# Kernel optimization log

Hardware: AMD Instinct MI355X
Metric: run time of the kernel (lower is better)

The kernel has to match this reference:

```python
import jax, jax.numpy as jnp
import numpy as np

E = 512      # moe_experts
M = 6        # per-expert dim = moe_dim // 2
H = 6        # moe_heads
D = 1024     # hidden_size
F = E * M    # flatten_shape = 3072

def relu2(x):
    return jnp.square(jax.nn.relu(x))

def setup_inputs() -> dict:
    key = jax.random.key(0)
    ks = jax.random.split(key, 12)
    B, S = 4, 2048
    inp = {
        "x": jax.random.normal(ks[0], (B, S, D), jnp.float32),
        "g1": jax.random.uniform(ks[1], (B, S, H, E), jnp.float32),
        "g2": jax.random.uniform(ks[2], (B, S, H, E), jnp.float32),
        "u1_w": jax.random.normal(ks[3], (F, D), jnp.float32) * 0.02,
        "u1_b": jnp.zeros((F,), jnp.float32),
        "u2_w": jax.random.normal(ks[4], (F, D), jnp.float32) * 0.02,
        "u2_b": jnp.zeros((F,), jnp.float32),
        "v11_w": jax.random.normal(ks[5], (D // 2, F), jnp.float32) * 0.02,
        "v12_w": jax.random.normal(ks[6], (D // 2, F), jnp.float32) * 0.02,
        "v21_w": jax.random.normal(ks[7], (D // 2, F), jnp.float32) * 0.02,
        "v22_w": jax.random.normal(ks[8], (D // 2, F), jnp.float32) * 0.02,
        "b1": jnp.zeros((E, D // 2), jnp.float32),
        "b2": jnp.zeros((E, D // 2), jnp.float32),
    }
    return inp

def reference(x, g1, g2, u1_w, u1_b, u2_w, u2_b, v11_w, v12_w, v21_w, v22_w, b1, b2):
    B, S, _ = x.shape
    # up-proj + relu^2, split into (experts E, per-expert dim M)
    x1 = relu2(x @ u1_w.T + u1_b).reshape(B, S, E, M)   # [B,S,E,M]
    x2 = relu2(x @ u2_w.T + u2_b).reshape(B, S, E, M)
    # gate sums over heads
    gs1 = jnp.einsum('bshi,bsim->bsim', g1, x1)          # sum_h g1 applied to x1
    gs2 = jnp.einsum('bshj,bsjm->bsjm', g2, x2)
    x11 = gs1.reshape(B, S, F) @ v11_w.T                 # [B,S,D/2]
    x22 = gs2.reshape(B, S, F) @ v22_w.T
    # cross terms: contract over h efficiently (avoid E x E materialization)
    t2 = jnp.einsum('bshj,bsjm->bshm', g2, x2)           # [B,S,H,M]
    x12 = jnp.einsum('bshm,bshi->bsim', t2, g1).reshape(B, S, F) @ v12_w.T
    t1 = jnp.einsum('bshi,bsim->bshm', g1, x1)
    x21 = jnp.einsum('bshm,bshj->bsjm', t1, g2).reshape(B, S, F) @ v21_w.T
    # bias terms through gates
    x13 = jnp.einsum('bshi,id->bsd', g1, b1)
    x23 = jnp.einsum('bshj,jd->bsd', g2, b2)
    return jnp.concatenate((x11 + x12 + x13, x21 + x22 + x23), axis=-1)
```

## Files before the change

kernel.cpp:

```cpp
#include <hip/hip_runtime.h>
#include <stdint.h>

typedef unsigned short u16;
typedef unsigned int u32;
typedef __attribute__((ext_vector_type(8))) short bf16x8;
typedef __attribute__((ext_vector_type(4))) float f32x4;

__device__ __forceinline__ float bf2f(u16 u) {
    unsigned v = ((unsigned)u) << 16;
    float f;
    __builtin_memcpy(&f, &v, 4);
    return f;
}
__device__ __forceinline__ u16 f2bf(float f) {
    unsigned x;
    __builtin_memcpy(&x, &f, 4);
    unsigned r = (x + 0x7fffu + ((x >> 16) & 1u)) >> 16;
    return (u16)r;
}

#define BM 128
#define BN 128
#define BK 32

#define GLDS(g, l) __builtin_amdgcn_global_load_lds( \
    (const __attribute__((address_space(1))) void*)(g), \
    (__attribute__((address_space(3))) void*)(l), 16, 0, 0)

__global__ __launch_bounds__(256) void gemm_bt(
    const u16* __restrict__ A0, const u16* __restrict__ A1, int lda,
    const u16* __restrict__ B0, const u16* __restrict__ B1, int ldb,
    const float* __restrict__ bias0, const float* __restrict__ bias1,
    u16* __restrict__ out0, u16* __restrict__ out1,
    int ldo, int colstep, int K)
{
    __shared__ __align__(16) u16 As[BM * BK];
    __shared__ __align__(16) u16 Bs[BN * BK];
    const int tid = threadIdx.x;
    const int z = blockIdx.z;
    const u16* A  = z ? A1 : A0;
    const u16* Bw = z ? B1 : B0;
    const int rowBase = blockIdx.y * BM;
    const int colBase = blockIdx.x * BN;
    const int wave = tid >> 6;
    const int lane = tid & 63;
    const int wm = (wave >> 1) * 64;
    const int wn = (wave & 1) * 64;
    const int mlane = lane & 15;
    const int quad  = lane >> 4;

    const int ca = tid;
    const int cb = tid + 256;
    const int ra = ca >> 2, sa = ca & 3;
    const int rb = cb >> 2, sb = cb & 3;
    const u16* gAa = A  + (size_t)(rowBase + ra) * lda + sa * 8;
    const u16* gAb = A  + (size_t)(rowBase + rb) * lda + sb * 8;
    const u16* gBa = Bw + (size_t)(colBase + ra) * ldb + sa * 8;
    const u16* gBb = Bw + (size_t)(colBase + rb) * ldb + sb * 8;

    f32x4 acc[4][4] = {};

    for (int k0 = 0; k0 < K; k0 += BK) {
        GLDS(gAa + k0, As + ca * 8);
        GLDS(gAb + k0, As + cb * 8);
        GLDS(gBa + k0, Bs + ca * 8);
        GLDS(gBb + k0, Bs + cb * 8);
        __syncthreads();
        bf16x8 af[4], bfr[4];
        #pragma unroll
        for (int t = 0; t < 4; ++t) {
            af[t]  = *(const bf16x8*)(As + (wm + t * 16 + mlane) * BK + quad * 8);
            bfr[t] = *(const bf16x8*)(Bs + (wn + t * 16 + mlane) * BK + quad * 8);
        }
        #pragma unroll
        for (int i = 0; i < 4; ++i)
            #pragma unroll
            for (int j = 0; j < 4; ++j)
                acc[i][j] = __builtin_amdgcn_mfma_f32_16x16x32_bf16(af[i], bfr[j], acc[i][j], 0, 0, 0);
        __syncthreads();
    }

    const float* bias = z ? bias1 : bias0;
    const int coloff = z * colstep;
    u16* outp = z ? out1 : out0;
    #pragma unroll
    for (int j = 0; j < 4; ++j) {
        const int col = colBase + wn + j * 16 + mlane;
        const float bv = bias[col];
        #pragma unroll
        for (int i = 0; i < 4; ++i) {
            const int rbse = rowBase + wm + i * 16 + quad * 4;
            #pragma unroll
            for (int r = 0; r < 4; ++r) {
                float v = acc[i][j][r] + bv;
                v = (v > 0.0f) ? v * v : 0.0f;
                outp[(size_t)(rbse + r) * ldo + coloff + col] = f2bf(v);
            }
        }
    }
}

__global__ __launch_bounds__(256) void gemm2_split(
    const u16* __restrict__ Y1, const u16* __restrict__ Y2,
    const u16* __restrict__ W1, const u16* __restrict__ W2,
    float* __restrict__ out, float* __restrict__ pbase, int nsplit)
{
    __shared__ __align__(16) u16 As[BM * BK];
    __shared__ __align__(16) u16 Bs[BN * BK];
    const int tid = threadIdx.x;
    const int z2cnt = 2 * nsplit;
    const int L = blockIdx.x;
    const int z2 = L % z2cnt;
    const int q  = L / z2cnt;
    const int bx = q & 3;
    const int by = q >> 2;
    const int z = z2 & 1;
    const int split = z2 >> 1;
    const int Ks = 6656 / nsplit;
    const int kbeg = split * Ks;

    const u16* A  = z ? Y2 : Y1;
    const u16* Bw = z ? W2 : W1;
    const int rowBase = by * BM;
    const int colBase = bx * BN;
    const int wave = tid >> 6;
    const int lane = tid & 63;
    const int wm = (wave >> 1) * 64;
    const int wn = (wave & 1) * 64;
    const int mlane = lane & 15;
    const int quad  = lane >> 4;

    const int ca = tid;
    const int cb = tid + 256;
    const int ra = ca >> 2, sa = ca & 3;
    const int rb = cb >> 2, sb = cb & 3;
    const u16* gAa = A  + (size_t)(rowBase + ra) * 6656 + sa * 8 + kbeg;
    const u16* gAb = A  + (size_t)(rowBase + rb) * 6656 + sb * 8 + kbeg;
    const u16* gBa = Bw + (size_t)(colBase + ra) * 6656 + sa * 8 + kbeg;
    const u16* gBb = Bw + (size_t)(colBase + rb) * 6656 + sb * 8 + kbeg;

    f32x4 acc[4][4] = {};

    for (int k0 = 0; k0 < Ks; k0 += BK) {
        GLDS(gAa + k0, As + ca * 8);
        GLDS(gAb + k0, As + cb * 8);
        GLDS(gBa + k0, Bs + ca * 8);
        GLDS(gBb + k0, Bs + cb * 8);
        __syncthreads();
        bf16x8 af[4], bfr[4];
        #pragma unroll
        for (int t = 0; t < 4; ++t) {
            af[t]  = *(const bf16x8*)(As + (wm + t * 16 + mlane) * BK + quad * 8);
            bfr[t] = *(const bf16x8*)(Bs + (wn + t * 16 + mlane) * BK + quad * 8);
        }
        #pragma unroll
        for (int i = 0; i < 4; ++i)
            #pragma unroll
            for (int j = 0; j < 4; ++j)
                acc[i][j] = __builtin_amdgcn_mfma_f32_16x16x32_bf16(af[i], bfr[j], acc[i][j], 0, 0, 0);
        __syncthreads();
    }

    float* dst = (split == 0) ? out : (pbase + (size_t)(split - 1) * 8192 * 1024);
    const int coloff = z * 512;
    #pragma unroll
    for (int j = 0; j < 4; ++j) {
        const int col = colBase + wn + j * 16 + mlane;
        #pragma unroll
        for (int i = 0; i < 4; ++i) {
            const int rbse = rowBase + wm + i * 16 + quad * 4;
            #pragma unroll
            for (int r = 0; r < 4; ++r)
                dst[(size_t)(rbse + r) * 1024 + coloff + col] = acc[i][j][r];
        }
    }
}

__global__ __launch_bounds__(256) void reduce_add(
    float4* __restrict__ out, const float4* __restrict__ p, int nadd)
{
    const int i = blockIdx.x * 256 + threadIdx.x;
    float4 v = out[i];
    for (int k = 0; k < nadd; ++k) {
        const float4 a = p[(size_t)k * 2097152 + i];
        v.x += a.x; v.y += a.y; v.z += a.z; v.w += a.w;
    }
    out[i] = v;
}

__global__ __launch_bounds__(256) void cvt_bf16(
    const float* __restrict__ x, const float* __restrict__ u1,
    const float* __restrict__ u2, u16* __restrict__ dst)
{
    const int idx4 = blockIdx.x * 256 + threadIdx.x;
    const int NX = 8388608 / 4, NU = 3145728 / 4;
    const float4* src;
    int off;
    if (idx4 < NX)           { src = (const float4*)x;  off = idx4; }
    else if (idx4 < NX + NU) { src = (const float4*)u1; off = idx4 - NX; }
    else                     { src = (const float4*)u2; off = idx4 - NX - NU; }
    const float4 v = src[off];
    ushort4 o;
    o.x = f2bf(v.x); o.y = f2bf(v.y); o.z = f2bf(v.z); o.w = f2bf(v.w);
    ((ushort4*)dst)[idx4] = o;
}

__global__ __launch_bounds__(256) void prep_wcat(
    const float* __restrict__ v11, const float* __restrict__ v12,
    const float* __restrict__ v21, const float* __restrict__ v22,
    const float* __restrict__ b1,  const float* __restrict__ b2,
    u16* __restrict__ W1, u16* __restrict__ W2)
{
    const int idx = blockIdx.x * 256 + threadIdx.x;
    const int n = idx / 6656;
    const int k = idx - n * 6656;
    float w1, w2;
    if (k < 3072)      { w1 = v11[n * 3072 + k];        w2 = v21[n * 3072 + k]; }
    else if (k < 6144) { w1 = v12[n * 3072 + k - 3072]; w2 = v22[n * 3072 + k - 3072]; }
    else               { w1 = b1[(k - 6144) * 512 + n]; w2 = b2[(k - 6144) * 512 + n]; }
    W1[idx] = f2bf(w1);
    W2[idx] = f2bf(w2);
}

__global__ __launch_bounds__(256) void gating(
    const float* __restrict__ g1, const float* __restrict__ g2,
    u16* __restrict__ Y1, u16* __restrict__ Y2)
{
    __shared__ __align__(16) u16 sm[17408];
    __shared__ float tls[72];
    u16* g1b = sm;
    u16* xT1 = sm + 3072;
    u16* g2b = sm + 6144;
    u16* xT2 = sm + 9216;
    const int tid = threadIdx.x;
    const int wave = tid >> 6, lane = tid & 63;
    const size_t tok = blockIdx.x;
    const size_t gb = tok * 3072;
    const size_t yb = tok * 6656;

    #pragma unroll
    for (int j = 0; j < 3; ++j) {
        const int c = tid + j * 256;
        float4 a = ((const float4*)(g1 + gb))[c];
        float4 b = ((const float4*)(g2 + gb))[c];
        ushort4 oa, ob;
        oa.x = f2bf(a.x); oa.y = f2bf(a.y); oa.z = f2bf(a.z); oa.w = f2bf(a.w);
        ob.x = f2bf(b.x); ob.y = f2bf(b.y); ob.z = f2bf(b.z); ob.w = f2bf(b.w);
        ((ushort4*)g1b)[c] = oa;
        ((ushort4*)g2b)[c] = ob;
        ushort4 xv1 = ((const ushort4*)(Y1 + yb))[c];
        ushort4 xv2 = ((const ushort4*)(Y2 + yb + 3072))[c];
        const u16 v1[4] = {xv1.x, xv1.y, xv1.z, xv1.w};
        const u16 v2[4] = {xv2.x, xv2.y, xv2.z, xv2.w};
        #pragma unroll
        for (int q = 0; q < 4; ++q) {
            const int e = c * 4 + q;
            const int i = e / 6;
            const int m = e - 6 * i;
            xT1[m * 512 + i] = v1[q];
            xT2[m * 512 + i] = v2[q];
        }
    }
    __syncthreads();

    if (wave < 2) {
        const u16* Ab = wave ? g2b : g1b;
        const u16* Bb = wave ? xT2 : xT1;
        const int fofs = (lane & 15) * 512 + (lane >> 4) * 8;
        f32x4 acc = {};
        #pragma unroll
        for (int k0 = 0; k0 < 512; k0 += 32) {
            bf16x8 af = *(const bf16x8*)(Ab + fofs + k0);
            bf16x8 bf = *(const bf16x8*)(Bb + fofs + k0);
            acc = __builtin_amdgcn_mfma_f32_16x16x32_bf16(af, bf, acc, 0, 0, 0);
        }
        const int col = lane & 15;
        const int rowb = (lane >> 4) * 4;
        float* ts = tls + wave * 36;
        #pragma unroll
        for (int r = 0; r < 4; ++r) {
            const int row = rowb + r;
            if (row < 6 && col < 6) ts[row * 6 + col] = acc[r];
        }
    }
    __syncthreads();

    const int t = tid;
    u32* Y1d = (u32*)(Y1 + yb);
    u32* Y2d = (u32*)(Y2 + yb);
    float sp1[2], sp2[2];
    #pragma unroll
    for (int e = 0; e < 2; ++e) {
        const int i = 2 * t + e;
        float g1v[6], g2v[6];
        float s1 = 0.f, s2 = 0.f;
        #pragma unroll
        for (int h = 0; h < 6; ++h) {
            g1v[h] = bf2f(g1b[h * 512 + i]); s1 += g1v[h];
            g2v[h] = bf2f(g2b[h * 512 + i]); s2 += g2v[h];
        }
        sp1[e] = s1; sp2[e] = s2;
        u32 pa1[3], pc2[3], pc1[3], pa2[3];
        #pragma unroll
        for (int mq = 0; mq < 3; ++mq) {
            u32 wa1 = 0, wc2 = 0, wc1 = 0, wa2 = 0;
            #pragma unroll
            for (int half = 0; half < 2; ++half) {
                const int m = mq * 2 + half;
                const float x1 = bf2f(xT1[m * 512 + i]);
                const float x2 = bf2f(xT2[m * 512 + i]);
                const float a1 = s1 * x1;
                const float a2 = s2 * x2;
                float c1 = 0.f, c2 = 0.f;
                #pragma unroll
                for (int h = 0; h < 6; ++h) {
                    c2 += tls[36 + h * 6 + m] * g1v[h];
                    c1 += tls[h * 6 + m] * g2v[h];
                }
                const int sh = half * 16;
                wa1 |= ((u32)f2bf(a1)) << sh;
                wc2 |= ((u32)f2bf(c2)) << sh;
                wc1 |= ((u32)f2bf(c1)) << sh;
                wa2 |= ((u32)f2bf(a2)) << sh;
            }
            pa1[mq] = wa1; pc2[mq] = wc2; pc1[mq] = wc1; pa2[mq] = wa2;
        }
        const int base = 6 * t + 3 * e;
        #pragma unroll
        for (int mq = 0; mq < 3; ++mq) {
            Y1d[base + mq]        = pa1[mq];
            Y1d[1536 + base + mq] = pc2[mq];
            Y2d[base + mq]        = pc1[mq];
            Y2d[1536 + base + mq] = pa2[mq];
        }
    }
    Y1d[3072 + t] = (u32)f2bf(sp1[0]) | (((u32)f2bf(sp1[1])) << 16);
    Y2d[3072 + t] = (u32)f2bf(sp2[0]) | (((u32)f2bf(sp2[1])) << 16);
}

extern "C" void kernel_launch(void* const* d_in, const int* in_sizes, int n_in,
                              void* d_out, int out_size, void* d_ws, size_t ws_size,
                              hipStream_t stream) {
    const float* x   = (const float*)d_in[0];
    const float* g1  = (const float*)d_in[1];
    const float* g2  = (const float*)d_in[2];
    const float* u1w = (const float*)d_in[3];
    const float* u1b = (const float*)d_in[4];
    const float* u2w = (const float*)d_in[5];
    const float* u2b = (const float*)d_in[6];
    const float* v11 = (const float*)d_in[7];
    const float* v12 = (const float*)d_in[8];
    const float* v21 = (const float*)d_in[9];
    const float* v22 = (const float*)d_in[10];
    const float* b1  = (const float*)d_in[11];
    const float* b2  = (const float*)d_in[12];
    float* out = (float*)d_out;

    u16* Y1   = (u16*)d_ws;
    u16* Y2   = Y1 + (size_t)8192 * 6656;
    u16* xbf  = Y2 + (size_t)8192 * 6656;
    u16* u1bf = xbf + (size_t)8192 * 1024;
    u16* u2bf = u1bf + (size_t)3072 * 1024;
    u16* W1   = u2bf + (size_t)3072 * 1024;
    u16* W2   = W1 + (size_t)512 * 6656;
    float* part = (float*)(W2 + (size_t)512 * 6656);

    const size_t base = (size_t)(W2 + (size_t)512 * 6656 - (u16*)d_ws) * 2;
    const size_t pbytes = (size_t)8192 * 1024 * 4;
    int nsplit = 1;
    if (ws_size >= base + 3 * pbytes) nsplit = 4;
    else if (ws_size >= base + pbytes) nsplit = 2;

    cvt_bf16<<<dim3(14336), 256, 0, stream>>>(x, u1w, u2w, xbf);
    prep_wcat<<<dim3(13312), 256, 0, stream>>>(v11, v12, v21, v22, b1, b2, W1, W2);

    gemm_bt<<<dim3(24, 64, 2), 256, 0, stream>>>(
        xbf, xbf, 1024, u1bf, u2bf, 1024, u1b, u2b, Y1, Y2, 6656, 3072, 1024);

    gating<<<dim3(8192), 256, 0, stream>>>(g1, g2, Y1, Y2);

    gemm2_split<<<dim3(4 * 64 * 2 * nsplit), 256, 0, stream>>>(
        Y1, Y2, W1, W2, out, part, nsplit);
    if (nsplit > 1)
        reduce_add<<<dim3(8192), 256, 0, stream>>>(
            (float4*)out, (const float4*)part, nsplit - 1);
}
```

Baseline: 669.8 us.

## Rewrite both GEMMs with 256x256 tiles, double-buffered swizzled LDS and phased MFMA

Both bf16 GEMMs move from a single-buffered 128x128 tile with BK=32 to a shared 512-thread 256x256 core with BK=64. The core uses two LDS buffers with XOR-swizzled rows, issues global-to-LDS loads for the next tiles between MFMA quarter-phases, and raises wave priority around the MFMA bursts. The aim is to hide memory latency behind compute, raise data reuse per loaded byte and avoid LDS bank conflicts. The second GEMM now splits K at most 2 ways, which means less partial traffic for the reduce step but fewer blocks to fill the GPU. The 128KB LDS footprint allows only one block per CU despite the launch bound, which reduces occupancy.

```diff
diff --git a/kernel.cpp b/kernel.cpp
--- a/kernel.cpp
+++ b/kernel.cpp
@@ -19,159 +19,189 @@
     return (u16)r;
 }
 
-#define BM 128
-#define BN 128
-#define BK 32
-
 #define GLDS(g, l) __builtin_amdgcn_global_load_lds( \
     (const __attribute__((address_space(1))) void*)(g), \
     (__attribute__((address_space(3))) void*)(l), 16, 0, 0)
 
-__global__ __launch_bounds__(256) void gemm_bt(
-    const u16* __restrict__ A0, const u16* __restrict__ A1, int lda,
-    const u16* __restrict__ B0, const u16* __restrict__ B1, int ldb,
-    const float* __restrict__ bias0, const float* __restrict__ bias1,
-    u16* __restrict__ out0, u16* __restrict__ out1,
-    int ldo, int colstep, int K)
-{
-    __shared__ __align__(16) u16 As[BM * BK];
-    __shared__ __align__(16) u16 Bs[BN * BK];
+#define BARX() do { asm volatile("" ::: "memory"); __builtin_amdgcn_s_barrier(); asm volatile("" ::: "memory"); } while (0)
+#define LGKM0() asm volatile("s_waitcnt lgkmcnt(0)" ::: "memory")
+#define WAIT_VM4() asm volatile("s_waitcnt vmcnt(4)" ::: "memory")
+#define WAIT_VM0() asm volatile("s_waitcnt vmcnt(0)" ::: "memory")
+
+__device__ __forceinline__ void gemm256_core(
+    const u16* gA, const u16* gB, size_t ldk, int NT,
+    u16* lds, int tid, f32x4 (&acc)[8][4])
+{
+    const int lane  = tid & 63;
+    const int wave  = tid >> 6;
+    const int wr    = wave >> 2;
+    const int wc    = wave & 3;
+    const int mlane = lane & 15;
+    const int quad  = lane >> 4;
+    const int swz   = mlane & 7;
+
+    u16* A0 = lds;
+    u16* B0 = lds + 16384;
+    u16* A1 = lds + 32768;
+    u16* B1 = lds + 49152;
+
+    #define ST_A(h, t, dst) do { \
+        GLDS(gA + (size_t)((h)*128     ) * ldk + (size_t)(t) * 64, (dst) + (h)*8192 + tid*8); \
+        GLDS(gA + (size_t)((h)*128 + 64) * ldk + (size_t)(t) * 64, (dst) + (h)*8192 + 4096 + tid*8); \
+    } while (0)
+    #define ST_B(h, t, dst) do { \
+        GLDS(gB + (size_t)((h)*128     ) * ldk + (size_t)(t) * 64, (dst) + (h)*8192 + tid*8); \
+        GLDS(gB + (size_t)((h)*128 + 64) * ldk + (size_t)(t) * 64, (dst) + (h)*8192 + 4096 + tid*8); \
+    } while (0)
+    #define RDA(mh) \
+        _Pragma("unroll") \
+        for (int m = 0; m < 4; ++m) { \
+            const int rA = wr*128 + ((mh)*4 + m)*16 + mlane; \
+            a[m][0] = *(const bf16x8*)(bA + rA*64 + (((0 + quad) ^ swz) * 8)); \
+            a[m][1] = *(const bf16x8*)(bA + rA*64 + (((4 + quad) ^ swz) * 8)); \
+        }
+    #define RDB(nh) \
+        _Pragma("unroll") \
+        for (int n = 0; n < 2; ++n) { \
+            const int rB = wc*64 + ((nh)*2 + n)*16 + mlane; \
+            b[(nh)*2 + n][0] = *(const bf16x8*)(bB + rB*64 + (((0 + quad) ^ swz) * 8)); \
+            b[(nh)*2 + n][1] = *(const bf16x8*)(bB + rB*64 + (((4 + quad) ^ swz) * 8)); \
+        }
+    #define MFMA_QUAD(MB, NB) do { \
+        __builtin_amdgcn_s_setprio(1); \
+        _Pragma("unroll") \
+        for (int m = 0; m < 4; ++m) \
+            _Pragma("unroll") \
+            for (int n = 0; n < 2; ++n) \
+                _Pragma("unroll") \
+                for (int k = 0; k < 2; ++k) \
+                    acc[(MB) + m][(NB) + n] = __builtin_amdgcn_mfma_f32_16x16x32_bf16( \
+                        a[m][k], b[(NB) + n][k], acc[(MB) + m][(NB) + n], 0, 0, 0); \
+        __builtin_amdgcn_s_setprio(0); \
+    } while (0)
+
+    ST_A(0, 0, A0); ST_A(1, 0, A0);
+    ST_B(0, 0, B0); ST_B(1, 0, B0);
+    ST_B(0, 1, B1); ST_B(1, 1, B1);
+    WAIT_VM4();
+    BARX();
+
+    bf16x8 a[4][2], b[4][2];
+
+    for (int u = 0; u < NT; ++u) {
+        u16* bA = (u & 1) ? A1 : A0;
+        u16* bB = (u & 1) ? B1 : B0;
+        u16* oA = (u & 1) ? A0 : A1;
+
+        RDA(0);
+        RDB(0);
+        if (u + 1 < NT) ST_A(0, u + 1, oA);
+        BARX(); LGKM0();
+        MFMA_QUAD(0, 0);
+        BARX();
+
+        RDB(1);
+        if (u + 1 < NT) ST_A(1, u + 1, oA);
+        BARX(); LGKM0();
+        MFMA_QUAD(0, 2);
+        BARX();
+
+        RDA(1);
+        if (u + 2 < NT) ST_B(0, u + 2, bB);
+        BARX(); LGKM0();
+        MFMA_QUAD(4, 2);
+        BARX();
+
+        if (u + 2 < NT) ST_B(1, u + 2, bB);
+        BARX(); LGKM0();
+        MFMA_QUAD(4, 0);
+        if (u + 2 < NT) { WAIT_VM4(); } else { WAIT_VM0(); }
+        BARX();
+    }
+    #undef ST_A
+    #undef ST_B
+    #undef RDA
+    #undef RDB
+    #undef MFMA_QUAD
+}
+
+__global__ __launch_bounds__(512, 2) void gemm1_8ph(
+    const u16* __restrict__ X, const u16* __restrict__ U1, const u16* __restrict__ U2,
+    const float* __restrict__ bias1, const float* __restrict__ bias2,
+    u16* __restrict__ Y1, u16* __restrict__ Y2)
+{
+    __shared__ __align__(16) u16 lds[65536];
     const int tid = threadIdx.x;
     const int z = blockIdx.z;
-    const u16* A  = z ? A1 : A0;
-    const u16* Bw = z ? B1 : B0;
-    const int rowBase = blockIdx.y * BM;
-    const int colBase = blockIdx.x * BN;
-    const int wave = tid >> 6;
-    const int lane = tid & 63;
-    const int wm = (wave >> 1) * 64;
-    const int wn = (wave & 1) * 64;
-    const int mlane = lane & 15;
-    const int quad  = lane >> 4;
-
-    const int ca = tid;
-    const int cb = tid + 256;
-    const int ra = ca >> 2, sa = ca & 3;
-    const int rb = cb >> 2, sb = cb & 3;
-    const u16* gAa = A  + (size_t)(rowBase + ra) * lda + sa * 8;
-    const u16* gAb = A  + (size_t)(rowBase + rb) * lda + sb * 8;
-    const u16* gBa = Bw + (size_t)(colBase + ra) * ldb + sa * 8;
-    const u16* gBb = Bw + (size_t)(colBase + rb) * ldb + sb * 8;
-
-    f32x4 acc[4][4] = {};
-
-    for (int k0 = 0; k0 < K; k0 += BK) {
-        GLDS(gAa + k0, As + ca * 8);
-        GLDS(gAb + k0, As + cb * 8);
-        GLDS(gBa + k0, Bs + ca * 8);
-        GLDS(gBb + k0, Bs + cb * 8);
-        __syncthreads();
-        bf16x8 af[4], bfr[4];
-        #pragma unroll
-        for (int t = 0; t < 4; ++t) {
-            af[t]  = *(const bf16x8*)(As + (wm + t * 16 + mlane) * BK + quad * 8);
-            bfr[t] = *(const bf16x8*)(Bs + (wn + t * 16 + mlane) * BK + quad * 8);
-        }
-        #pragma unroll
-        for (int i = 0; i < 4; ++i)
-            #pragma unroll
-            for (int j = 0; j < 4; ++j)
-                acc[i][j] = __builtin_amdgcn_mfma_f32_16x16x32_bf16(af[i], bfr[j], acc[i][j], 0, 0, 0);
-        __syncthreads();
-    }
-
-    const float* bias = z ? bias1 : bias0;
-    const int coloff = z * colstep;
-    u16* outp = z ? out1 : out0;
+    const int rowBase = blockIdx.y * 256;
+    const int colBase = blockIdx.x * 256;
+    const int r0 = tid >> 3;
+    const int cs = ((tid & 7) ^ (r0 & 7)) * 8;
+    const u16* gA = X + (size_t)(rowBase + r0) * 1024 + cs;
+    const u16* gB = (z ? U2 : U1) + (size_t)(colBase + r0) * 1024 + cs;
+
+    f32x4 acc[8][4] = {};
+    gemm256_core(gA, gB, 1024, 16, lds, tid, acc);
+
+    const float* bias = z ? bias2 : bias1;
+    u16* outp = z ? Y2 : Y1;
+    const int coloff = z * 3072;
+    const int lane = tid & 63, wave = tid >> 6;
+    const int wr = wave >> 2, wc = wave & 3;
+    const int mlane = lane & 15, quad = lane >> 4;
     #pragma unroll
-    for (int j = 0; j < 4; ++j) {
-        const int col = colBase + wn + j * 16 + mlane;
+    for (int n = 0; n < 4; ++n) {
+        const int col = colBase + wc * 64 + n * 16 + mlane;
         const float bv = bias[col];
         #pragma unroll
-        for (int i = 0; i < 4; ++i) {
-            const int rbse = rowBase + wm + i * 16 + quad * 4;
+        for (int m = 0; m < 8; ++m) {
+            const int rb = rowBase + wr * 128 + m * 16 + quad * 4;
             #pragma unroll
             for (int r = 0; r < 4; ++r) {
-                float v = acc[i][j][r] + bv;
+                float v = acc[m][n][r] + bv;
                 v = (v > 0.0f) ? v * v : 0.0f;
-                outp[(size_t)(rbse + r) * ldo + coloff + col] = f2bf(v);
+                outp[(size_t)(rb + r) * 6656 + coloff + col] = f2bf(v);
             }
         }
     }
 }
 
-__global__ __launch_bounds__(256) void gemm2_split(
+__global__ __launch_bounds__(512, 2) void gemm2_8ph(
     const u16* __restrict__ Y1, const u16* __restrict__ Y2,
     const u16* __restrict__ W1, const u16* __restrict__ W2,
-    float* __restrict__ out, float* __restrict__ pbase, int nsplit)
-{
-    __shared__ __align__(16) u16 As[BM * BK];
-    __shared__ __align__(16) u16 Bs[BN * BK];
+    float* __restrict__ out, float* __restrict__ part, int nsplit)
+{
+    __shared__ __align__(16) u16 lds[65536];
     const int tid = threadIdx.x;
-    const int z2cnt = 2 * nsplit;
-    const int L = blockIdx.x;
-    const int z2 = L % z2cnt;
-    const int q  = L / z2cnt;
-    const int bx = q & 3;
-    const int by = q >> 2;
+    const int z2 = blockIdx.z;
     const int z = z2 & 1;
     const int split = z2 >> 1;
     const int Ks = 6656 / nsplit;
     const int kbeg = split * Ks;
-
-    const u16* A  = z ? Y2 : Y1;
-    const u16* Bw = z ? W2 : W1;
-    const int rowBase = by * BM;
-    const int colBase = bx * BN;
-    const int wave = tid >> 6;
-    const int lane = tid & 63;
-    const int wm = (wave >> 1) * 64;
-    const int wn = (wave & 1) * 64;
-    const int mlane = lane & 15;
-    const int quad  = lane >> 4;
-
-    const int ca = tid;
-    const int cb = tid + 256;
-    const int ra = ca >> 2, sa = ca & 3;
-    const int rb = cb >> 2, sb = cb & 3;
-    const u16* gAa = A  + (size_t)(rowBase + ra) * 6656 + sa * 8 + kbeg;
-    const u16* gAb = A  + (size_t)(rowBase + rb) * 6656 + sb * 8 + kbeg;
-    const u16* gBa = Bw + (size_t)(colBase + ra) * 6656 + sa * 8 + kbeg;
-    const u16* gBb = Bw + (size_t)(colBase + rb) * 6656 + sb * 8 + kbeg;
-
-    f32x4 acc[4][4] = {};
-
-    for (int k0 = 0; k0 < Ks; k0 += BK) {
-        GLDS(gAa + k0, As + ca * 8);
-        GLDS(gAb + k0, As + cb * 8);
-        GLDS(gBa + k0, Bs + ca * 8);
-        GLDS(gBb + k0, Bs + cb * 8);
-        __syncthreads();
-        bf16x8 af[4], bfr[4];
-        #pragma unroll
-        for (int t = 0; t < 4; ++t) {
-            af[t]  = *(const bf16x8*)(As + (wm + t * 16 + mlane) * BK + quad * 8);
-            bfr[t] = *(const bf16x8*)(Bs + (wn + t * 16 + mlane) * BK + quad * 8);
-        }
-        #pragma unroll
-        for (int i = 0; i < 4; ++i)
-            #pragma unroll
-            for (int j = 0; j < 4; ++j)
-                acc[i][j] = __builtin_amdgcn_mfma_f32_16x16x32_bf16(af[i], bfr[j], acc[i][j], 0, 0, 0);
-        __syncthreads();
-    }
-
-    float* dst = (split == 0) ? out : (pbase + (size_t)(split - 1) * 8192 * 1024);
+    const int rowBase = blockIdx.y * 256;
+    const int colBase = blockIdx.x * 256;
+    const int r0 = tid >> 3;
+    const int cs = ((tid & 7) ^ (r0 & 7)) * 8;
+    const u16* gA = (z ? Y2 : Y1) + (size_t)(rowBase + r0) * 6656 + kbeg + cs;
+    const u16* gB = (z ? W2 : W1) + (size_t)(colBase + r0) * 6656 + kbeg + cs;
+
+    f32x4 acc[8][4] = {};
+    gemm256_core(gA, gB, 6656, Ks >> 6, lds, tid, acc);
+
+    float* dst = split ? part : out;
     const int coloff = z * 512;
+    const int lane = tid & 63, wave = tid >> 6;
+    const int wr = wave >> 2, wc = wave & 3;
+    const int mlane = lane & 15, quad = lane >> 4;
     #pragma unroll
-    for (int j = 0; j < 4; ++j) {
-        const int col = colBase + wn + j * 16 + mlane;
-        #pragma unroll
-        for (int i = 0; i < 4; ++i) {
-            const int rbse = rowBase + wm + i * 16 + quad * 4;
+    for (int n = 0; n < 4; ++n) {
+        const int col = colBase + wc * 64 + n * 16 + mlane;
+        #pragma unroll
+        for (int m = 0; m < 8; ++m) {
+            const int rb = rowBase + wr * 128 + m * 16 + quad * 4;
             #pragma unroll
             for (int r = 0; r < 4; ++r)
-                dst[(size_t)(rbse + r) * 1024 + coloff + col] = acc[i][j][r];
+                dst[(size_t)(rb + r) * 1024 + coloff + col] = acc[m][n][r];
         }
     }
 }
@@ -242,10 +272,10 @@
     for (int j = 0; j < 3; ++j) {
         const int c = tid + j * 256;
         float4 a = ((const float4*)(g1 + gb))[c];
-        float4 b = ((const float4*)(g2 + gb))[c];
+        float4 bq = ((const float4*)(g2 + gb))[c];
         ushort4 oa, ob;
         oa.x = f2bf(a.x); oa.y = f2bf(a.y); oa.z = f2bf(a.z); oa.w = f2bf(a.w);
-        ob.x = f2bf(b.x); ob.y = f2bf(b.y); ob.z = f2bf(b.z); ob.w = f2bf(b.w);
+        ob.x = f2bf(bq.x); ob.y = f2bf(bq.y); ob.z = f2bf(bq.z); ob.w = f2bf(bq.w);
         ((ushort4*)g1b)[c] = oa;
         ((ushort4*)g2b)[c] = ob;
         ushort4 xv1 = ((const ushort4*)(Y1 + yb))[c];
@@ -367,19 +397,17 @@
 
     const size_t base = (size_t)(W2 + (size_t)512 * 6656 - (u16*)d_ws) * 2;
     const size_t pbytes = (size_t)8192 * 1024 * 4;
-    int nsplit = 1;
-    if (ws_size >= base + 3 * pbytes) nsplit = 4;
-    else if (ws_size >= base + pbytes) nsplit = 2;
+    const int nsplit = (ws_size >= base + pbytes) ? 2 : 1;
 
     cvt_bf16<<<dim3(14336), 256, 0, stream>>>(x, u1w, u2w, xbf);
     prep_wcat<<<dim3(13312), 256, 0, stream>>>(v11, v12, v21, v22, b1, b2, W1, W2);
 
-    gemm_bt<<<dim3(24, 64, 2), 256, 0, stream>>>(
-        xbf, xbf, 1024, u1bf, u2bf, 1024, u1b, u2b, Y1, Y2, 6656, 3072, 1024);
+    gemm1_8ph<<<dim3(12, 32, 2), 512, 0, stream>>>(
+        xbf, u1bf, u2bf, u1b, u2b, Y1, Y2);
 
     gating<<<dim3(8192), 256, 0, stream>>>(g1, g2, Y1, Y2);
 
-    gemm2_split<<<dim3(4 * 64 * 2 * nsplit), 256, 0, stream>>>(
+    gemm2_8ph<<<dim3(2, 32, 2 * nsplit), 512, 0, stream>>>(
         Y1, Y2, W1, W2, out, part, nsplit);
     if (nsplit > 1)
         reduce_add<<<dim3(8192), 256, 0, stream>>>(
```

Measured after the change: 586.2 us. 1.14x faster.
